# Performance work log

Measured on AMD Instinct MI355X. Metric: run time of the kernel, lower is better.

The kernel has to match this reference:

```python
import jax, jax.numpy as jnp
import numpy as np

B, T, C = 8, 2048, 1024
DK = 64  # d_k = n_embd // n_head = 1024 // 16


def setup_inputs() -> dict:
    key = jax.random.key(0)
    ks = jax.random.split(key, 4)
    X = jax.random.normal(ks[0], (B, T, C), dtype=jnp.float32)
    scale = 1.0 / np.sqrt(C)
    Wq = jax.random.normal(ks[1], (C, DK), dtype=jnp.float32) * scale
    Wk = jax.random.normal(ks[2], (C, DK), dtype=jnp.float32) * scale
    Wv = jax.random.normal(ks[3], (C, DK), dtype=jnp.float32) * scale
    bq = jnp.zeros((DK,), dtype=jnp.float32)
    bk = jnp.zeros((DK,), dtype=jnp.float32)
    bv = jnp.zeros((DK,), dtype=jnp.float32)
    return {"X": X, "Wq": Wq, "bq": bq, "Wk": Wk, "bk": bk, "Wv": Wv, "bv": bv}


def reference(X, Wq, bq, Wk, bk, Wv, bv):
    # Single-head causal self-attention (dropout disabled / eval mode).
    T_ = X.shape[1]
    Q = X @ Wq + bq  # [B, T, d_k]
    K = X @ Wk + bk
    V = X @ Wv + bv
    scores = jnp.einsum('btd,bsd->bts', Q, K) / jnp.sqrt(jnp.float32(Q.shape[-1]))
    causal = jnp.tril(jnp.ones((T_, T_), dtype=bool))  # tril mask
    scores = jnp.where(causal, scores, -jnp.inf)
    weights = jax.nn.softmax(scores, axis=-1)
    out = jnp.einsum('bts,bsd->btd', weights, V)  # [B, T, d_k]
    return out
```

## Files before the change

kernel.cpp:

```cpp
#include <hip/hip_runtime.h>
#include <math.h>

#define NB 8
#define NT 2048
#define NC 1024
#define DK 64
#define BT (NB*NT)

#define QKV_BYTES  (3u * BT * DK * 2u)
#define SLOT_BYTES 8704u

typedef unsigned short ushort_t;
typedef unsigned int uint_t;
typedef __attribute__((ext_vector_type(8))) short short8;
typedef __attribute__((ext_vector_type(4))) float f32x4;

__device__ __forceinline__ float bf2f(uint_t u) {
    union { uint_t i; float f; } v;
    v.i = u << 16;
    return v.f;
}
__device__ __forceinline__ ushort_t f2bf(float f) {
    union { float f; uint_t i; } v; v.f = f;
    uint_t x = v.i;
    return (ushort_t)((x + 0x7fffu + ((x >> 16) & 1u)) >> 16);
}
__device__ __forceinline__ uint_t pack2bf(float lo, float hi) {
    return (uint_t)f2bf(lo) | ((uint_t)f2bf(hi) << 16);
}

__device__ __forceinline__ int seg_prefix(int qt) {
    const int a = qt >> 2;
    return 2 * a * (a + 1) - 4 + (qt & 3) * (a + 1);
}

__global__ __launch_bounds__(256) void wt_prep_kernel(
    const float* __restrict__ Wq, const float* __restrict__ Wk,
    const float* __restrict__ Wv, ushort_t* __restrict__ WtG)
{
    const int tg = blockIdx.x * 256 + threadIdx.x;
    const int n  = tg >> 7;
    const int k0 = (tg & 127) * 8;
    const float* W = (n < 64) ? Wq : (n < 128) ? Wk : Wv;
    const int nc = n & 63;
    ushort_t o[8];
    #pragma unroll
    for (int j = 0; j < 8; ++j) o[j] = f2bf(W[(size_t)(k0 + j) * DK + nc]);
    *reinterpret_cast<uint4*>(&WtG[n * NC + k0]) = *reinterpret_cast<uint4*>(o);
}

__global__ __launch_bounds__(256, 2) void qkv_mfma_kernel(
    const float* __restrict__ X, const ushort_t* __restrict__ WtG,
    const float* __restrict__ bq, const float* __restrict__ bk,
    const float* __restrict__ bv, ushort_t* __restrict__ QKV)
{
    __shared__ ushort_t Xs[2][32 * 72];
    __shared__ ushort_t VtL[64 * 40];

    const int t    = threadIdx.x;
    const int w    = t >> 6;
    const int lane = t & 63;
    const int g    = lane >> 4;
    const int col  = lane & 15;
    const int m0   = blockIdx.x * 32;

    const int xrow = t >> 3;
    const int xc   = (t & 7) * 8;

    float xf[8];
    short8 wA[6], wB[6];

    auto LOADX = [&](int k0) {
        const float4* xp = reinterpret_cast<const float4*>(
            &X[(size_t)(m0 + xrow) * NC + k0 + xc]);
        float4 v0 = xp[0], v1 = xp[1];
        xf[0] = v0.x; xf[1] = v0.y; xf[2] = v0.z; xf[3] = v0.w;
        xf[4] = v1.x; xf[5] = v1.y; xf[6] = v1.z; xf[7] = v1.w;
    };
    auto LOADW = [&](int k0, short8* wn) {
        #pragma unroll
        for (int tj = 0; tj < 3; ++tj) {
            const int ng = 48 * w + 16 * tj + col;
            #pragma unroll
            for (int c = 0; c < 2; ++c)
                wn[tj * 2 + c] = *reinterpret_cast<const short8*>(
                    &WtG[ng * NC + k0 + 32 * c + 8 * g]);
        }
    };
    auto WRITEX = [&](int b) {
        ushort_t xb[8];
        #pragma unroll
        for (int j = 0; j < 8; ++j) xb[j] = f2bf(xf[j]);
        *reinterpret_cast<uint4*>(&Xs[b][xrow * 72 + xc]) =
            *reinterpret_cast<uint4*>(xb);
    };

    f32x4 acc[2][3];
    #pragma unroll
    for (int ri = 0; ri < 2; ++ri)
        #pragma unroll
        for (int tj = 0; tj < 3; ++tj) acc[ri][tj] = (f32x4){0.f, 0.f, 0.f, 0.f};

    auto COMPUTE = [&](int cur, short8* wc) {
        const ushort_t* XsB = Xs[cur];
        #pragma unroll
        for (int c = 0; c < 2; ++c) {
            short8 af[2];
            #pragma unroll
            for (int ri = 0; ri < 2; ++ri)
                af[ri] = *reinterpret_cast<const short8*>(
                    &XsB[(16 * ri + col) * 72 + 32 * c + 8 * g]);
            #pragma unroll
            for (int ri = 0; ri < 2; ++ri)
                #pragma unroll
                for (int tj = 0; tj < 3; ++tj)
                    acc[ri][tj] = __builtin_amdgcn_mfma_f32_16x16x32_bf16(
                        af[ri], wc[tj * 2 + c], acc[ri][tj], 0, 0, 0);
        }
    };

    LOADX(0);
    LOADW(0, wA);
    WRITEX(0);

    #pragma unroll
    for (int ks2 = 0; ks2 < 8; ++ks2) {
        {
            const int ks = 2 * ks2;
            if (ks < 15) { LOADX((ks + 1) * 64); LOADW((ks + 1) * 64, wB); }
            __syncthreads();
            COMPUTE(0, wA);
            if (ks < 15) WRITEX(1);
        }
        {
            const int ks = 2 * ks2 + 1;
            if (ks < 15) { LOADX((ks + 1) * 64); LOADW((ks + 1) * 64, wA); }
            __syncthreads();
            COMPUTE(1, wB);
            if (ks < 15) WRITEX(0);
        }
    }

    #pragma unroll
    for (int tj = 0; tj < 3; ++tj) {
        const int ng    = 48 * w + 16 * tj + col;
        const int which = ng >> 6, ncol = ng & 63;
        const float* bp = (which == 0) ? bq : (which == 1) ? bk : bv;
        const float bb  = bp[ncol];
        if (which == 2) {
            #pragma unroll
            for (int ri = 0; ri < 2; ++ri)
                #pragma unroll
                for (int r = 0; r < 4; ++r)
                    VtL[ncol * 40 + 16 * ri + 4 * g + r] = f2bf(acc[ri][tj][r] + bb);
        } else {
            const float qs = (which == 0) ? 0.125f : 1.0f;
            ushort_t* Y = QKV + (size_t)which * BT * DK;
            #pragma unroll
            for (int ri = 0; ri < 2; ++ri)
                #pragma unroll
                for (int r = 0; r < 4; ++r) {
                    const int rowg = m0 + 16 * ri + 4 * g + r;
                    Y[(size_t)rowg * DK + ncol] = f2bf((acc[ri][tj][r] + bb) * qs);
                }
        }
    }
    __syncthreads();
    {
        ushort_t* Vt = QKV + (size_t)2 * BT * DK;
        const int d   = t >> 2;
        const int sg  = t & 3;
        uint4 v = *reinterpret_cast<const uint4*>(&VtL[d * 40 + sg * 8]);
        *reinterpret_cast<uint4*>(&Vt[(size_t)d * BT + m0 + sg * 8]) = v;
    }
}

__global__ __launch_bounds__(256) void attn_seg_kernel(
    const ushort_t* __restrict__ QKV, float* __restrict__ Out,
    char* __restrict__ Pbase)
{
    const ushort_t* Qw = QKV;
    const ushort_t* Kw = QKV + (size_t)BT * DK;
    const ushort_t* Vw = QKV + (size_t)2 * BT * DK;

    __shared__ ushort_t Ks[256 * 72];
    __shared__ ushort_t VtL[64 * 288];

    const int t     = threadIdx.x;
    const int w     = t >> 6;
    const int lane  = t & 63;
    const int g     = lane >> 4;
    const int col   = lane & 15;
    const int batch = blockIdx.x & 7;
    const int u     = blockIdx.x >> 3;

    int s;
    if      (u < 16) s = 0;
    else if (u < 30) s = 1;
    else if (u < 42) s = 2;
    else if (u < 52) s = 3;
    else if (u < 60) s = 4;
    else if (u < 66) s = 5;
    else if (u < 70) s = 6;
    else             s = 7;
    const int off2 = 16 * s - s * (s - 1);
    const int qt0  = 4 * s + 2 * (u - off2);
    const int kbase = 256 * s;

    {
        const int sr = t >> 2;
        const int ss = t & 3;
        #pragma unroll
        for (int i = 0; i < 4; ++i) {
            const int krow = 64 * i + sr;
            const size_t gk = ((size_t)(batch * NT) + kbase + krow) * DK + ss * 16;
            const uint4* kp = reinterpret_cast<const uint4*>(Kw + gk);
            *reinterpret_cast<uint4*>(&Ks[krow * 72 + ss * 16])     = kp[0];
            *reinterpret_cast<uint4*>(&Ks[krow * 72 + ss * 16 + 8]) = kp[1];
            const size_t gv = (size_t)sr * BT + (batch * NT + kbase + 64 * i) + ss * 16;
            const uint4* vp = reinterpret_cast<const uint4*>(Vw + gv);
            *reinterpret_cast<uint4*>(&VtL[sr * 288 + 72 * i + ss * 16])     = vp[0];
            *reinterpret_cast<uint4*>(&VtL[sr * 288 + 72 * i + ss * 16 + 8]) = vp[1];
        }
    }
    __syncthreads();

    #pragma unroll
    for (int iq = 0; iq < 2; ++iq) {
        const int qt   = qt0 + iq;
        const int qrow = qt * 64 + 16 * w + col;
        const int kcnt = min(4, qt - 4 * s + 1);
        const int diag = qt - 4 * s;

        short8 qf0, qf1;
        {
            const ushort_t* Qrow = Qw + ((size_t)(batch * NT) + qrow) * DK;
            qf0 = *reinterpret_cast<const short8*>(Qrow + 8 * g);
            qf1 = *reinterpret_cast<const short8*>(Qrow + 32 + 8 * g);
        }

        f32x4 Oa[4];
        #pragma unroll
        for (int dt = 0; dt < 4; ++dt) Oa[dt] = (f32x4){0.f, 0.f, 0.f, 0.f};
        float m = -INFINITY, l = 0.0f;

        for (int ktl = 0; ktl < kcnt; ++ktl) {
            f32x4 sa[4];
            #pragma unroll
            for (int tj = 0; tj < 4; ++tj) sa[tj] = (f32x4){0.f, 0.f, 0.f, 0.f};
            #pragma unroll
            for (int tj = 0; tj < 4; ++tj) {
                const ushort_t* kb = &Ks[(64 * ktl + col + 16 * tj) * 72 + 8 * g];
                short8 kf0 = *reinterpret_cast<const short8*>(kb);
                short8 kf1 = *reinterpret_cast<const short8*>(kb + 32);
                sa[tj] = __builtin_amdgcn_mfma_f32_16x16x32_bf16(kf0, qf0, sa[tj], 0, 0, 0);
                sa[tj] = __builtin_amdgcn_mfma_f32_16x16x32_bf16(kf1, qf1, sa[tj], 0, 0, 0);
            }

            float sv[4][4];
            #pragma unroll
            for (int tj = 0; tj < 4; ++tj)
                #pragma unroll
                for (int r = 0; r < 4; ++r) sv[tj][r] = sa[tj][r];

            if (ktl == diag) {
                const int s0 = (kbase + 64 * ktl);
                #pragma unroll
                for (int tj = 0; tj < 4; ++tj)
                    #pragma unroll
                    for (int r = 0; r < 4; ++r)
                        if (s0 + 16 * tj + 4 * g + r > qrow) sv[tj][r] = -INFINITY;
            }

            float vmax = sv[0][0];
            #pragma unroll
            for (int tj = 0; tj < 4; ++tj)
                #pragma unroll
                for (int r = 0; r < 4; ++r) vmax = fmaxf(vmax, sv[tj][r]);
            vmax = fmaxf(vmax, __shfl_xor(vmax, 16, 64));
            vmax = fmaxf(vmax, __shfl_xor(vmax, 32, 64));

            const float mn = fmaxf(m, vmax);
            const float sc = __expf(m - mn);
            m = mn;

            float p[4][4];
            float lt = 0.f;
            #pragma unroll
            for (int tj = 0; tj < 4; ++tj)
                #pragma unroll
                for (int r = 0; r < 4; ++r) {
                    p[tj][r] = __expf(sv[tj][r] - mn);
                    lt += p[tj][r];
                }
            lt += __shfl_xor(lt, 16, 64);
            lt += __shfl_xor(lt, 32, 64);
            l = l * sc + lt;

            float sco[4];
            #pragma unroll
            for (int r = 0; r < 4; ++r) sco[r] = __shfl(sc, 20 * g + r, 64);
            #pragma unroll
            for (int dt = 0; dt < 4; ++dt)
                #pragma unroll
                for (int r = 0; r < 4; ++r) Oa[dt][r] *= sco[r];

            uint_t pk0[4], pk1[4];
            #pragma unroll
            for (int tj = 0; tj < 4; ++tj) {
                pk0[tj] = pack2bf(p[tj][0], p[tj][1]);
                pk1[tj] = pack2bf(p[tj][2], p[tj][3]);
            }
            const int sA = col + 32 * (g & 1);
            const int sB = sA + 16;
            const bool hi = (g >= 2);

            #pragma unroll
            for (int c = 0; c < 2; ++c) {
                uint_t w0a = __shfl(pk0[2*c], sA, 64), w0b = __shfl(pk0[2*c+1], sA, 64);
                uint_t w1a = __shfl(pk1[2*c], sA, 64), w1b = __shfl(pk1[2*c+1], sA, 64);
                uint_t w2a = __shfl(pk0[2*c], sB, 64), w2b = __shfl(pk0[2*c+1], sB, 64);
                uint_t w3a = __shfl(pk1[2*c], sB, 64), w3b = __shfl(pk1[2*c+1], sB, 64);
                uint_t pa[4];
                pa[0] = hi ? w0b : w0a;
                pa[1] = hi ? w1b : w1a;
                pa[2] = hi ? w2b : w2a;
                pa[3] = hi ? w3b : w3a;
                short8 paf = *reinterpret_cast<const short8*>(pa);
                #pragma unroll
                for (int dt = 0; dt < 4; ++dt) {
                    short8 vf = *reinterpret_cast<const short8*>(
                        &VtL[(col + 16 * dt) * 288 + 72 * ktl + 32 * c + 8 * g]);
                    Oa[dt] = __builtin_amdgcn_mfma_f32_16x16x32_bf16(paf, vf, Oa[dt], 0, 0, 0);
                }
            }
        }

        float lr[4];
        #pragma unroll
        for (int r = 0; r < 4; ++r) lr[r] = __shfl(l, 20 * g + r, 64);

        if (qt < 4) {
            #pragma unroll
            for (int r = 0; r < 4; ++r) {
                const float inv = 1.0f / lr[r];
                const int row = qt * 64 + 16 * w + 4 * g + r;
                float* op = Out + ((size_t)(batch * NT) + row) * DK + col;
                #pragma unroll
                for (int dt = 0; dt < 4; ++dt) op[16 * dt] = Oa[dt][r] * inv;
            }
        } else {
            float mr[4];
            #pragma unroll
            for (int r = 0; r < 4; ++r) mr[r] = __shfl(m, 20 * g + r, 64);
            const int slot = batch * 140 + seg_prefix(qt) + s;
            char* sp = Pbase + (size_t)slot * SLOT_BYTES;
            ushort_t* Ob  = reinterpret_cast<ushort_t*>(sp);
            float*    Pm  = reinterpret_cast<float*>(sp + 8192);
            float*    Plv = reinterpret_cast<float*>(sp + 8448);
            #pragma unroll
            for (int r = 0; r < 4; ++r) {
                const int rloc = 16 * w + 4 * g + r;
                #pragma unroll
                for (int dt = 0; dt < 4; ++dt)
                    Ob[rloc * 64 + 16 * dt + col] = f2bf(Oa[dt][r]);
                if (col == 0) { Pm[rloc] = mr[r]; Plv[rloc] = lr[r]; }
            }
        }
    }
}

__global__ __launch_bounds__(256) void attn_combine_kernel(
    const char* __restrict__ Pbase, float* __restrict__ Out)
{
    const int bid   = blockIdx.x;
    const int batch = bid / 28;
    const int qt    = 4 + bid % 28;
    const int nseg  = (qt >> 2) + 1;
    const int slot0 = batch * 140 + seg_prefix(qt);

    const int t   = threadIdx.x;
    const int row = t >> 2;
    const int d0  = (t & 3) * 16;

    float ms[8], ls[8];
    float M = -INFINITY;
    #pragma unroll
    for (int s = 0; s < 8; ++s)
        if (s < nseg) {
            const char* sp = Pbase + (size_t)(slot0 + s) * SLOT_BYTES;
            ms[s] = reinterpret_cast<const float*>(sp + 8192)[row];
            ls[s] = reinterpret_cast<const float*>(sp + 8448)[row];
            M = fmaxf(M, ms[s]);
        }

    float acc[16];
    #pragma unroll
    for (int j = 0; j < 16; ++j) acc[j] = 0.f;
    float ltot = 0.f;

    #pragma unroll
    for (int s = 0; s < 8; ++s)
        if (s < nseg) {
            const float wsc = __expf(ms[s] - M);
            ltot += wsc * ls[s];
            const ushort_t* Ob = reinterpret_cast<const ushort_t*>(
                Pbase + (size_t)(slot0 + s) * SLOT_BYTES) + row * 64 + d0;
            uint4 u0 = *reinterpret_cast<const uint4*>(Ob);
            uint4 u1 = *reinterpret_cast<const uint4*>(Ob + 8);
            const uint_t* uu = reinterpret_cast<const uint_t*>(&u0);
            #pragma unroll
            for (int j = 0; j < 4; ++j) {
                acc[2*j+0] += wsc * bf2f(uu[j] & 0xffffu);
                acc[2*j+1] += wsc * bf2f(uu[j] >> 16);
            }
            const uint_t* uv = reinterpret_cast<const uint_t*>(&u1);
            #pragma unroll
            for (int j = 0; j < 4; ++j) {
                acc[8+2*j+0] += wsc * bf2f(uv[j] & 0xffffu);
                acc[8+2*j+1] += wsc * bf2f(uv[j] >> 16);
            }
        }

    const float inv = 1.0f / ltot;
    float* op = Out + ((size_t)(batch * NT) + qt * 64 + row) * DK + d0;
    #pragma unroll
    for (int j = 0; j < 16; ++j) op[j] = acc[j] * inv;
}

extern "C" void kernel_launch(void* const* d_in, const int* in_sizes, int n_in,
                              void* d_out, int out_size, void* d_ws, size_t ws_size,
                              hipStream_t stream) {
    const float* X  = (const float*)d_in[0];
    const float* Wq = (const float*)d_in[1];
    const float* bq = (const float*)d_in[2];
    const float* Wk = (const float*)d_in[3];
    const float* bk = (const float*)d_in[4];
    const float* Wv = (const float*)d_in[5];
    const float* bv = (const float*)d_in[6];
    float* Out = (float*)d_out;
    ushort_t* QKV = (ushort_t*)d_ws;
    char* Pbase   = (char*)d_ws + QKV_BYTES;
    ushort_t* WtG = (ushort_t*)d_out;

    wt_prep_kernel<<<96, 256, 0, stream>>>(Wq, Wk, Wv, WtG);
    qkv_mfma_kernel<<<512, 256, 0, stream>>>(X, WtG, bq, bk, bv, QKV);
    attn_seg_kernel<<<576, 256, 0, stream>>>(QKV, Out, Pbase);
    attn_combine_kernel<<<224, 256, 0, stream>>>(Pbase, Out);
}
```

Before: 66.04 us.

## Split QKV projection K-dimension across two warp groups and skip unused K tiles

The QKV projection kernel now runs 512 threads per block. Two 256-thread groups each handle half of the 1024-wide reduction and combine their partial accumulators through shared memory before the epilogue. This doubles the in-flight loads per block and halves the serial K loop, at the cost of extra LDS, an additional reduction step and sync. The attention kernel also loads only the K/V tiles that causal segments actually need, instead of always loading four.

After: 66.12 us. About the same (+0.1%).

```diff
diff --git a/kernel.cpp b/kernel.cpp
--- a/kernel.cpp
+++ b/kernel.cpp
@@ -49,30 +49,34 @@
     *reinterpret_cast<uint4*>(&WtG[n * NC + k0]) = *reinterpret_cast<uint4*>(o);
 }
 
-__global__ __launch_bounds__(256, 2) void qkv_mfma_kernel(
+__global__ __launch_bounds__(512, 4) void qkv_mfma_kernel(
     const float* __restrict__ X, const ushort_t* __restrict__ WtG,
     const float* __restrict__ bq, const float* __restrict__ bk,
     const float* __restrict__ bv, ushort_t* __restrict__ QKV)
 {
-    __shared__ ushort_t Xs[2][32 * 72];
+    __shared__ ushort_t Xs[2][2][32 * 72];
+    __shared__ float    Racc[32 * 196];
     __shared__ ushort_t VtL[64 * 40];
 
     const int t    = threadIdx.x;
-    const int w    = t >> 6;
+    const int grp  = t >> 8;
+    const int tg   = t & 255;
+    const int w    = (t >> 6) & 3;
     const int lane = t & 63;
     const int g    = lane >> 4;
     const int col  = lane & 15;
     const int m0   = blockIdx.x * 32;
-
-    const int xrow = t >> 3;
-    const int xc   = (t & 7) * 8;
+    const int kb   = grp * 512;
+
+    const int xrow = tg >> 3;
+    const int xc   = (tg & 7) * 8;
 
     float xf[8];
     short8 wA[6], wB[6];
 
     auto LOADX = [&](int k0) {
         const float4* xp = reinterpret_cast<const float4*>(
-            &X[(size_t)(m0 + xrow) * NC + k0 + xc]);
+            &X[(size_t)(m0 + xrow) * NC + kb + k0 + xc]);
         float4 v0 = xp[0], v1 = xp[1];
         xf[0] = v0.x; xf[1] = v0.y; xf[2] = v0.z; xf[3] = v0.w;
         xf[4] = v1.x; xf[5] = v1.y; xf[6] = v1.z; xf[7] = v1.w;
@@ -84,14 +88,14 @@
             #pragma unroll
             for (int c = 0; c < 2; ++c)
                 wn[tj * 2 + c] = *reinterpret_cast<const short8*>(
-                    &WtG[ng * NC + k0 + 32 * c + 8 * g]);
+                    &WtG[ng * NC + kb + k0 + 32 * c + 8 * g]);
         }
     };
     auto WRITEX = [&](int b) {
         ushort_t xb[8];
         #pragma unroll
         for (int j = 0; j < 8; ++j) xb[j] = f2bf(xf[j]);
-        *reinterpret_cast<uint4*>(&Xs[b][xrow * 72 + xc]) =
+        *reinterpret_cast<uint4*>(&Xs[grp][b][xrow * 72 + xc]) =
             *reinterpret_cast<uint4*>(xb);
     };
 
@@ -102,7 +106,7 @@
         for (int tj = 0; tj < 3; ++tj) acc[ri][tj] = (f32x4){0.f, 0.f, 0.f, 0.f};
 
     auto COMPUTE = [&](int cur, short8* wc) {
-        const ushort_t* XsB = Xs[cur];
+        const ushort_t* XsB = Xs[grp][cur];
         #pragma unroll
         for (int c = 0; c < 2; ++c) {
             short8 af[2];
@@ -124,52 +128,75 @@
     WRITEX(0);
 
     #pragma unroll
-    for (int ks2 = 0; ks2 < 8; ++ks2) {
+    for (int ks2 = 0; ks2 < 4; ++ks2) {
         {
             const int ks = 2 * ks2;
-            if (ks < 15) { LOADX((ks + 1) * 64); LOADW((ks + 1) * 64, wB); }
+            if (ks < 7) { LOADX((ks + 1) * 64); LOADW((ks + 1) * 64, wB); }
             __syncthreads();
             COMPUTE(0, wA);
-            if (ks < 15) WRITEX(1);
+            if (ks < 7) WRITEX(1);
         }
         {
             const int ks = 2 * ks2 + 1;
-            if (ks < 15) { LOADX((ks + 1) * 64); LOADW((ks + 1) * 64, wA); }
+            if (ks < 7) { LOADX((ks + 1) * 64); LOADW((ks + 1) * 64, wA); }
             __syncthreads();
             COMPUTE(1, wB);
-            if (ks < 15) WRITEX(0);
-        }
-    }
-
-    #pragma unroll
-    for (int tj = 0; tj < 3; ++tj) {
-        const int ng    = 48 * w + 16 * tj + col;
-        const int which = ng >> 6, ncol = ng & 63;
-        const float* bp = (which == 0) ? bq : (which == 1) ? bk : bv;
-        const float bb  = bp[ncol];
-        if (which == 2) {
-            #pragma unroll
-            for (int ri = 0; ri < 2; ++ri)
+            if (ks < 7) WRITEX(0);
+        }
+    }
+
+    __syncthreads();
+    if (grp == 1) {
+        #pragma unroll
+        for (int ri = 0; ri < 2; ++ri)
+            #pragma unroll
+            for (int tj = 0; tj < 3; ++tj)
                 #pragma unroll
                 for (int r = 0; r < 4; ++r)
-                    VtL[ncol * 40 + 16 * ri + 4 * g + r] = f2bf(acc[ri][tj][r] + bb);
-        } else {
-            const float qs = (which == 0) ? 0.125f : 1.0f;
-            ushort_t* Y = QKV + (size_t)which * BT * DK;
-            #pragma unroll
-            for (int ri = 0; ri < 2; ++ri)
-                #pragma unroll
-                for (int r = 0; r < 4; ++r) {
-                    const int rowg = m0 + 16 * ri + 4 * g + r;
-                    Y[(size_t)rowg * DK + ncol] = f2bf((acc[ri][tj][r] + bb) * qs);
-                }
-        }
+                    Racc[(16 * ri + 4 * g + r) * 196 + 48 * w + 16 * tj + col] =
+                        acc[ri][tj][r];
     }
     __syncthreads();
-    {
+    if (grp == 0) {
+        #pragma unroll
+        for (int ri = 0; ri < 2; ++ri)
+            #pragma unroll
+            for (int tj = 0; tj < 3; ++tj)
+                #pragma unroll
+                for (int r = 0; r < 4; ++r)
+                    acc[ri][tj][r] +=
+                        Racc[(16 * ri + 4 * g + r) * 196 + 48 * w + 16 * tj + col];
+
+        #pragma unroll
+        for (int tj = 0; tj < 3; ++tj) {
+            const int ng    = 48 * w + 16 * tj + col;
+            const int which = ng >> 6, ncol = ng & 63;
+            const float* bp = (which == 0) ? bq : (which == 1) ? bk : bv;
+            const float bb  = bp[ncol];
+            if (which == 2) {
+                #pragma unroll
+                for (int ri = 0; ri < 2; ++ri)
+                    #pragma unroll
+                    for (int r = 0; r < 4; ++r)
+                        VtL[ncol * 40 + 16 * ri + 4 * g + r] = f2bf(acc[ri][tj][r] + bb);
+            } else {
+                const float qs = (which == 0) ? 0.125f : 1.0f;
+                ushort_t* Y = QKV + (size_t)which * BT * DK;
+                #pragma unroll
+                for (int ri = 0; ri < 2; ++ri)
+                    #pragma unroll
+                    for (int r = 0; r < 4; ++r) {
+                        const int rowg = m0 + 16 * ri + 4 * g + r;
+                        Y[(size_t)rowg * DK + ncol] = f2bf((acc[ri][tj][r] + bb) * qs);
+                    }
+            }
+        }
+    }
+    __syncthreads();
+    if (grp == 0) {
         ushort_t* Vt = QKV + (size_t)2 * BT * DK;
-        const int d   = t >> 2;
-        const int sg  = t & 3;
+        const int d  = tg >> 2;
+        const int sg = tg & 3;
         uint4 v = *reinterpret_cast<const uint4*>(&VtL[d * 40 + sg * 8]);
         *reinterpret_cast<uint4*>(&Vt[(size_t)d * BT + m0 + sg * 8]) = v;
     }
@@ -206,12 +233,12 @@
     const int off2 = 16 * s - s * (s - 1);
     const int qt0  = 4 * s + 2 * (u - off2);
     const int kbase = 256 * s;
+    const int ntile = min(4, qt0 + 2 - 4 * s);
 
     {
         const int sr = t >> 2;
         const int ss = t & 3;
-        #pragma unroll
-        for (int i = 0; i < 4; ++i) {
+        for (int i = 0; i < ntile; ++i) {
             const int krow = 64 * i + sr;
             const size_t gk = ((size_t)(batch * NT) + kbase + krow) * DK + ss * 16;
             const uint4* kp = reinterpret_cast<const uint4*>(Kw + gk);
@@ -444,7 +471,7 @@
     ushort_t* WtG = (ushort_t*)d_out;
 
     wt_prep_kernel<<<96, 256, 0, stream>>>(Wq, Wk, Wv, WtG);
-    qkv_mfma_kernel<<<512, 256, 0, stream>>>(X, WtG, bq, bk, bv, QKV);
+    qkv_mfma_kernel<<<512, 512, 0, stream>>>(X, WtG, bq, bk, bv, QKV);
     attn_seg_kernel<<<576, 256, 0, stream>>>(QKV, Out, Pbase);
     attn_combine_kernel<<<224, 256, 0, stream>>>(Pbase, Out);
 }
```
